# Performance work log

Hardware: AMD Instinct MI355X
Metric: run time of the kernel (lower is better)

## Reference

```python
import jax, jax.numpy as jnp
import numpy as np


def _linear_init(key, fan_in, fan_out):
    k1, k2 = jax.random.split(key)
    sc = 1.0 / np.sqrt(fan_in)
    w = jax.random.uniform(k1, (fan_in, fan_out), jnp.float32, -sc, sc)
    b = jax.random.uniform(k2, (fan_out,), jnp.float32, -sc, sc)
    return w, b


def setup_inputs() -> dict:
    key = jax.random.key(0)
    ks = jax.random.split(key, 16)
    b, s, q, c, d = 8, 5, 15, 256, 4
    inp = {
        'support_xf': jax.random.normal(ks[0], (b, s, c, d, d), jnp.float32),
        'query_xf': jax.random.normal(ks[1], (b, q, c, d, d), jnp.float32),
        'support_y': jax.random.randint(ks[2], (b, s), 0, 5),
        'query_y': jax.random.randint(ks[3], (b, q), 0, 5),
    }
    g_dims = [(516, 256), (256, 256), (256, 256), (256, 256)]
    for i, (fi, fo) in enumerate(g_dims):
        w, bb = _linear_init(ks[4 + i], fi, fo)
        inp['g_w%d' % (i + 1)] = w
        inp['g_b%d' % (i + 1)] = bb
    f_dims = [(256, 256), (256, 256), (256, 29), (29, 1)]
    for i, (fi, fo) in enumerate(f_dims):
        w, bb = _linear_init(ks[8 + i], fi, fo)
        inp['f_w%d' % (i + 1)] = w
        inp['f_b%d' % (i + 1)] = bb
    return inp


def reference(support_xf, query_xf, support_y, query_y,
              g_w1, g_b1, g_w2, g_b2, g_w3, g_b3, g_w4, g_b4,
              f_w1, f_b1, f_w2, f_b2, f_w3, f_b3, f_w4, f_b4):
    b, s, c, d, _ = support_xf.shape
    q = query_xf.shape[1]
    d2 = d * d
    relu = jax.nn.relu
    # coord channels: ch0 = i/d (row), ch1 = j/d (col), shape [2, d, d]
    ii = jnp.arange(d, dtype=support_xf.dtype) / d
    coord = jnp.stack([jnp.broadcast_to(ii[:, None], (d, d)),
                       jnp.broadcast_to(ii[None, :], (d, d))], axis=0)
    sup = jnp.concatenate([support_xf, jnp.broadcast_to(coord, (b, s, 2, d, d))], axis=2)
    qry = jnp.concatenate([query_xf, jnp.broadcast_to(coord, (b, q, 2, d, d))], axis=2)
    cp = c + 2
    sup = sup.reshape(b, s, cp, d2).transpose(0, 1, 3, 2)  # [b,s,d2,cp]
    qry = qry.reshape(b, q, cp, d2).transpose(0, 1, 3, 2)  # [b,q,d2,cp]
    # pair[b,q,s,m,n] = concat(support feature at spatial n, query feature at spatial m)
    sup_e = jnp.broadcast_to(sup[:, None, :, None, :, :], (b, q, s, d2, d2, cp))
    qry_e = jnp.broadcast_to(qry[:, :, None, :, None, :], (b, q, s, d2, d2, cp))
    x = jnp.concatenate([sup_e, qry_e], axis=-1)  # [b,q,s,d2,d2,2*cp]
    # g MLP applied per pair
    x = relu(x @ g_w1 + g_b1)
    x = relu(x @ g_w2 + g_b2)
    x = relu(x @ g_w3 + g_b3)
    x = relu(x @ g_w4 + g_b4)
    xf = x.sum(axis=(3, 4))  # sum over d^4 pairs -> [b,q,s,256]
    # f MLP (Dropout is identity in eval mode)
    y = relu(xf @ f_w1 + f_b1)
    y = relu(y @ f_w2 + f_b2)
    y = relu(y @ f_w3 + f_b3)
    score = jax.nn.sigmoid(y @ f_w4 + f_b4)[..., 0]  # [b,q,s]
    label = (support_y[:, None, :] == query_y[:, :, None]).astype(score.dtype)
    loss = jnp.sum((label - score) ** 2) / b
    return loss
```

## Files before the change

### kernel.cpp

```cpp
#include <hip/hip_runtime.h>

typedef __attribute__((ext_vector_type(8))) __bf16 bf16x8;
typedef __attribute__((ext_vector_type(8))) short short8;
typedef __attribute__((ext_vector_type(4))) float f32x4;
typedef unsigned int u32;

static __device__ __forceinline__ unsigned short f2bf(float f) {
    u32 u = __float_as_uint(f);
    u += 0x7FFFu + ((u >> 16) & 1u);
    return (unsigned short)(u >> 16);
}
static __device__ __forceinline__ u32 cvt_pk_bf16(float lo, float hi) {
    u32 r;
    asm("v_cvt_pk_bf16_f32 %0, %1, %2" : "=v"(r) : "v"(lo), "v"(hi));
    return r;
}
static __device__ __forceinline__ bf16x8 as_bf16x8(short8 v) {
    return __builtin_bit_cast(bf16x8, v);
}
static __device__ __forceinline__ f32x4 mfma16(short8 a, short8 b, f32x4 c) {
    return __builtin_amdgcn_mfma_f32_16x16x32_bf16(as_bf16x8(a), as_bf16x8(b), c, 0, 0, 0);
}

#define NB 8
#define NS 5
#define NQ 15
#define A_OFF_F 0
#define B_OFF_F (640*256)
#define XF_OFF_F (B_OFF_F + 1920*256)
#define WF_OFF_BYTES ((XF_OFF_F + 600*1024)*4)
#define WF1_OFF_BYTES (WF_OFF_BYTES + 48*8192)

__global__ void kA(const float* __restrict__ w2, const float* __restrict__ w3,
                   const float* __restrict__ w4, const float* __restrict__ w1,
                   unsigned short* __restrict__ wf, unsigned short* __restrict__ wf1) {
    int bid = blockIdx.x;
    int l = threadIdx.x;
    if (bid < 48) {
        int L = bid >> 4, tt = bid & 15;
        const float* W = (L == 0) ? w2 : ((L == 1) ? w3 : w4);
        int nn = tt * 16 + (l & 15);
        #pragma unroll
        for (int kk = 0; kk < 8; ++kk) {
            int k0 = kk * 32 + (l >> 4) * 8;
            short8 ov;
            #pragma unroll
            for (int j = 0; j < 8; ++j)
                ov[j] = (short)f2bf(W[(size_t)(k0 + j) * 256 + nn]);
            *(short8*)((char*)wf + (size_t)bid * 8192 + kk * 1024 + l * 16) = ov;
        }
        return;
    }
    int c1 = bid - 48;
    int S = c1 >> 4, tt = c1 & 15;
    int nn = tt * 16 + (l & 15);
    for (int kk = 0; kk < 9; ++kk) {
        int k0 = kk * 32 + (l >> 4) * 8;
        short8 ov;
        #pragma unroll
        for (int j = 0; j < 8; ++j) {
            int kb = k0 + j;
            float v = (kb < 258) ? w1[(size_t)(S * 258 + kb) * 256 + nn] : 0.0f;
            ov[j] = (short)f2bf(v);
        }
        *(short8*)((char*)wf1 + (size_t)c1 * 9216 + kk * 1024 + l * 16) = ov;
    }
}

__launch_bounds__(512, 1)
__global__ void kB(const float* __restrict__ sup, const float* __restrict__ qry,
                   const unsigned short* __restrict__ wf1,
                   const float* __restrict__ gb1, float* __restrict__ ws) {
    __shared__ short Xf[18432];
    int bid = blockIdx.x;
    bool isA = (bid < 10);
    int S = isA ? 0 : 1;
    int cellbase = isA ? bid * 4 : (bid - 10) * 4;
    const float* src = isA ? sup : qry;
    float* dst0 = ws + (isA ? A_OFF_F : B_OFF_F);
    int t = threadIdx.x;
    int w = t >> 6, l = t & 63;
    int g = l >> 4, c = l & 15;
    char* Xb = (char*)Xf;
    const char* w1b = (const char*)wf1;

    for (int idx = w; idx < 36; idx += 8) {
        int m = idx / 9, kk = idx % 9;
        const float* xp = src + (size_t)(cellbase + m) * 4096;
        int kbase = kk * 32 + g * 8;
        float v[8];
        #pragma unroll
        for (int j = 0; j < 8; ++j) {
            int kb = kbase + j;
            float x;
            if (kb < 256)       x = xp[(size_t)kb * 16 + c];
            else if (kb == 256) x = (float)(c >> 2) * 0.25f;
            else if (kb == 257) x = (float)(c & 3) * 0.25f;
            else                x = 0.0f;
            v[j] = x;
        }
        uint4 hv;
        hv.x = cvt_pk_bf16(v[0], v[1]);
        hv.y = cvt_pk_bf16(v[2], v[3]);
        hv.z = cvt_pk_bf16(v[4], v[5]);
        hv.w = cvt_pk_bf16(v[6], v[7]);
        *(uint4*)(Xb + (size_t)(m * 9 + kk) * 1024 + l * 16) = hv;
    }
    __syncthreads();

    int wp = w >> 2, wn = w & 3;
    const char* wbase = w1b + (size_t)(S * 16 + wn * 4) * 9216;
    short8 wcur[4];
    #pragma unroll
    for (int tti = 0; tti < 4; ++tti)
        wcur[tti] = *(const short8*)(wbase + (size_t)tti * 9216 + l * 16);

    f32x4 acc[2][4];
    #pragma unroll
    for (int pg = 0; pg < 2; ++pg)
        #pragma unroll
        for (int tti = 0; tti < 4; ++tti)
            acc[pg][tti] = (f32x4){0.f, 0.f, 0.f, 0.f};

    #pragma unroll
    for (int kk = 0; kk < 9; ++kk) {
        int kn = kk + 1; if (kn > 8) kn = 8;
        short8 wnxt[4];
        #pragma unroll
        for (int tti = 0; tti < 4; ++tti)
            wnxt[tti] = *(const short8*)(wbase + (size_t)tti * 9216 + kn * 1024 + l * 16);
        #pragma unroll
        for (int pg = 0; pg < 2; ++pg) {
            short8 h = *(const short8*)(Xb + (size_t)((wp * 2 + pg) * 9 + kk) * 1024 + l * 16);
            #pragma unroll
            for (int tti = 0; tti < 4; ++tti)
                acc[pg][tti] = mfma16(wcur[tti], h, acc[pg][tti]);
        }
        #pragma unroll
        for (int tti = 0; tti < 4; ++tti) wcur[tti] = wnxt[tti];
    }

    #pragma unroll
    for (int tti = 0; tti < 4; ++tti) {
        int col0 = wn * 64 + tti * 16 + g * 4;
        float4 bv = {0.f, 0.f, 0.f, 0.f};
        if (S == 0) bv = *(const float4*)(gb1 + col0);
        #pragma unroll
        for (int pg = 0; pg < 2; ++pg) {
            int row = (cellbase + wp * 2 + pg) * 16 + c;
            float4 o;
            o.x = acc[pg][tti][0] + bv.x;
            o.y = acc[pg][tti][1] + bv.y;
            o.z = acc[pg][tti][2] + bv.z;
            o.w = acc[pg][tti][3] + bv.w;
            *(float4*)(dst0 + (size_t)row * 256 + col0) = o;
        }
    }
}

__launch_bounds__(512, 4)
__global__ void k3_g(const float* __restrict__ wsA, const float* __restrict__ wsB,
                     const unsigned short* __restrict__ wf,
                     const float* __restrict__ gb2, const float* __restrict__ gb3,
                     const float* __restrict__ gb4, float* __restrict__ xf) {
    __shared__ short Hf[32768];
    __shared__ float bs[768];
    int bid = blockIdx.x;
    int bqs = bid >> 1, half = bid & 1;
    int b = bqs / 75, rem = bqs % 75, qi = rem / 5, si = rem % 5;
    int t = threadIdx.x;
    int w = t >> 6, l = t & 63;
    int g = l >> 4, c = l & 15;
    int wp = w >> 2, wn = w & 3;
    char* Hb = (char*)Hf;
    const char* wfb = (const char*)wf;

    if (t < 256) { bs[t] = gb2[t]; bs[256 + t] = gb3[t]; bs[512 + t] = gb4[t]; }

    short8 wcur[4];
    #pragma unroll
    for (int tti = 0; tti < 4; ++tti)
        wcur[tti] = *(const short8*)(wfb + (size_t)(wn * 4 + tti) * 8192 + l * 16);

    {
        const float* Arow = wsA + (size_t)(b * NS + si) * 4096 + c * 256;
        const float* Brow = wsB + (size_t)(b * NQ + qi) * 4096 + (half * 8 + w) * 256;
        #pragma unroll
        for (int kk = 0; kk < 8; ++kk) {
            const float* ap = Arow + kk * 32 + g * 8;
            const float* bp = Brow + kk * 32 + g * 8;
            float4 a0 = *(const float4*)ap, a1 = *(const float4*)(ap + 4);
            float4 b0 = *(const float4*)bp, b1 = *(const float4*)(bp + 4);
            uint4 hv;
            hv.x = cvt_pk_bf16(fmaxf(a0.x + b0.x, 0.f), fmaxf(a0.y + b0.y, 0.f));
            hv.y = cvt_pk_bf16(fmaxf(a0.z + b0.z, 0.f), fmaxf(a0.w + b0.w, 0.f));
            hv.z = cvt_pk_bf16(fmaxf(a1.x + b1.x, 0.f), fmaxf(a1.y + b1.y, 0.f));
            hv.w = cvt_pk_bf16(fmaxf(a1.z + b1.z, 0.f), fmaxf(a1.w + b1.w, 0.f));
            *(uint4*)(Hb + (size_t)(w * 8 + kk) * 1024 + l * 16) = hv;
        }
    }
    __syncthreads();

    #pragma unroll 1
    for (int L = 0; L < 3; ++L) {
        f32x4 acc[4][4];
        #pragma unroll
        for (int pg = 0; pg < 4; ++pg)
            #pragma unroll
            for (int tti = 0; tti < 4; ++tti)
                acc[pg][tti] = (f32x4){0.f, 0.f, 0.f, 0.f};

        #pragma unroll
        for (int kk = 0; kk < 8; ++kk) {
            int s = L * 8 + kk + 1; if (s > 23) s = 23;
            int Ln = s >> 3, kn = s & 7;
            short8 wnxt[4];
            #pragma unroll
            for (int tti = 0; tti < 4; ++tti)
                wnxt[tti] = *(const short8*)(wfb +
                    (size_t)(Ln * 16 + wn * 4 + tti) * 8192 + kn * 1024 + l * 16);
            #pragma unroll
            for (int pg = 0; pg < 4; ++pg) {
                short8 h = *(const short8*)(Hb +
                    (size_t)((wp * 4 + pg) * 8 + kk) * 1024 + l * 16);
                #pragma unroll
                for (int tti = 0; tti < 4; ++tti)
                    acc[pg][tti] = mfma16(wcur[tti], h, acc[pg][tti]);
            }
            #pragma unroll
            for (int tti = 0; tti < 4; ++tti) wcur[tti] = wnxt[tti];
        }

        float4 bv[4];
        #pragma unroll
        for (int tti = 0; tti < 4; ++tti)
            bv[tti] = *(const float4*)(bs + L * 256 + wn * 64 + tti * 16 + g * 4);

        if (L < 2) {
            __syncthreads();
            #pragma unroll
            for (int pg = 0; pg < 4; ++pg) {
                int m = wp * 4 + pg;
                #pragma unroll
                for (int tti = 0; tti < 4; ++tti) {
                    uint2 q;
                    q.x = cvt_pk_bf16(fmaxf(acc[pg][tti][0] + bv[tti].x, 0.f),
                                      fmaxf(acc[pg][tti][1] + bv[tti].y, 0.f));
                    q.y = cvt_pk_bf16(fmaxf(acc[pg][tti][2] + bv[tti].z, 0.f),
                                      fmaxf(acc[pg][tti][3] + bv[tti].w, 0.f));
                    int kk2 = wn * 2 + (tti >> 1);
                    int dlane = ((tti & 1) * 2 + (g >> 1)) * 16 + c;
                    *(uint2*)(Hb + (size_t)(m * 8 + kk2) * 1024 + dlane * 16 + (g & 1) * 8) = q;
                }
            }
            __syncthreads();
        } else {
            #pragma unroll
            for (int tti = 0; tti < 4; ++tti) {
                float s0 = 0.f, s1 = 0.f, s2 = 0.f, s3 = 0.f;
                #pragma unroll
                for (int pg = 0; pg < 4; ++pg) {
                    s0 += fmaxf(acc[pg][tti][0] + bv[tti].x, 0.f);
                    s1 += fmaxf(acc[pg][tti][1] + bv[tti].y, 0.f);
                    s2 += fmaxf(acc[pg][tti][2] + bv[tti].z, 0.f);
                    s3 += fmaxf(acc[pg][tti][3] + bv[tti].w, 0.f);
                }
                #pragma unroll
                for (int d = 1; d < 16; d <<= 1) {
                    s0 += __shfl_xor(s0, d); s1 += __shfl_xor(s1, d);
                    s2 += __shfl_xor(s2, d); s3 += __shfl_xor(s3, d);
                }
                if (c == 0) {
                    float4 o = {s0, s1, s2, s3};
                    *(float4*)(xf + (((size_t)bqs * 2 + half) * 2 + wp) * 256 +
                               wn * 64 + tti * 16 + g * 4) = o;
                }
            }
        }
    }
}

__global__ void k4_f(const float* __restrict__ xf,
                     const float* __restrict__ fw1, const float* __restrict__ fb1,
                     const float* __restrict__ fw2, const float* __restrict__ fb2,
                     const float* __restrict__ fw3, const float* __restrict__ fb3,
                     const float* __restrict__ fw4, const float* __restrict__ fb4,
                     const int* __restrict__ sy, const int* __restrict__ qy,
                     float* __restrict__ out) {
    __shared__ float xb[4][256], yb[4][256], y3[4][32];
    int base = blockIdx.x * 4;
    int t = threadIdx.x;
    #pragma unroll
    for (int cc = 0; cc < 4; ++cc) {
        const float* xr = xf + (size_t)(base + cc) * 1024 + t;
        xb[cc][t] = xr[0] + xr[256] + xr[512] + xr[768];
    }
    __syncthreads();
    float acc[4];
    #pragma unroll
    for (int cc = 0; cc < 4; ++cc) acc[cc] = fb1[t];
    #pragma unroll 8
    for (int k = 0; k < 256; ++k) {
        float wv = fw1[(size_t)k * 256 + t];
        #pragma unroll
        for (int cc = 0; cc < 4; ++cc) acc[cc] += xb[cc][k] * wv;
    }
    #pragma unroll
    for (int cc = 0; cc < 4; ++cc) yb[cc][t] = acc[cc] > 0.f ? acc[cc] : 0.f;
    __syncthreads();
    #pragma unroll
    for (int cc = 0; cc < 4; ++cc) acc[cc] = fb2[t];
    #pragma unroll 8
    for (int k = 0; k < 256; ++k) {
        float wv = fw2[(size_t)k * 256 + t];
        #pragma unroll
        for (int cc = 0; cc < 4; ++cc) acc[cc] += yb[cc][k] * wv;
    }
    #pragma unroll
    for (int cc = 0; cc < 4; ++cc) xb[cc][t] = acc[cc] > 0.f ? acc[cc] : 0.f;
    __syncthreads();
    if (t < 116) {
        int cc = t / 29, col = t % 29;
        float a = fb3[col];
        #pragma unroll 8
        for (int k = 0; k < 256; ++k) a += xb[cc][k] * fw3[(size_t)k * 29 + col];
        y3[cc][col] = a > 0.f ? a : 0.f;
    }
    __syncthreads();
    if (t < 4) {
        int cc = t;
        float z = fb4[0];
        for (int k = 0; k < 29; ++k) z += y3[cc][k] * fw4[k];
        float score = 1.0f / (1.0f + __expf(-z));
        int bqs = base + cc;
        int b = bqs / 75, rem = bqs % 75, qi = rem / 5, si = rem % 5;
        float label = (sy[b * NS + si] == qy[b * NQ + qi]) ? 1.0f : 0.0f;
        float d = label - score;
        atomicAdd(out, d * d * 0.125f);
    }
}

extern "C" void kernel_launch(void* const* d_in, const int* in_sizes, int n_in,
                              void* d_out, int out_size, void* d_ws, size_t ws_size,
                              hipStream_t stream) {
    const float* sup = (const float*)d_in[0];
    const float* qry = (const float*)d_in[1];
    const int*   sy  = (const int*)d_in[2];
    const int*   qy  = (const int*)d_in[3];
    const float* gw1 = (const float*)d_in[4];
    const float* gb1 = (const float*)d_in[5];
    const float* gw2 = (const float*)d_in[6];
    const float* gb2 = (const float*)d_in[7];
    const float* gw3 = (const float*)d_in[8];
    const float* gb3 = (const float*)d_in[9];
    const float* gw4 = (const float*)d_in[10];
    const float* gb4 = (const float*)d_in[11];
    const float* fw1 = (const float*)d_in[12];
    const float* fb1 = (const float*)d_in[13];
    const float* fw2 = (const float*)d_in[14];
    const float* fb2 = (const float*)d_in[15];
    const float* fw3 = (const float*)d_in[16];
    const float* fb3 = (const float*)d_in[17];
    const float* fw4 = (const float*)d_in[18];
    const float* fb4 = (const float*)d_in[19];

    float* ws = (float*)d_ws;
    float* A  = ws + A_OFF_F;
    float* B  = ws + B_OFF_F;
    float* xf = ws + XF_OFF_F;
    unsigned short* wf  = (unsigned short*)((char*)d_ws + WF_OFF_BYTES);
    unsigned short* wf1 = (unsigned short*)((char*)d_ws + WF1_OFF_BYTES);
    float* out = (float*)d_out;

    hipMemsetAsync(out, 0, sizeof(float), stream);

    kA<<<80, 64, 0, stream>>>(gw2, gw3, gw4, gw1, wf, wf1);
    kB<<<40, 512, 0, stream>>>(sup, qry, wf1, gb1, ws);
    k3_g<<<1200, 512, 0, stream>>>(A, B, wf, gb2, gb3, gb4, xf);
    k4_f<<<150, 256, 0, stream>>>(xf, fw1, fb1, fw2, fb2, fw3, fb3, fw4, fb4, sy, qy, out);
}
```

Before: 126.0 us.

## Split g-MLP blocks into quarters with double-buffered weights and MFMA priority

Result: no change. 127.6 us (+1.3%).

```diff
diff --git a/kernel.cpp b/kernel.cpp
--- a/kernel.cpp
+++ b/kernel.cpp
@@ -158,33 +158,55 @@
     }
 }
 
-__launch_bounds__(512, 4)
+#define K3_STEP(CUR, NXT, KK)                                                   \
+    {                                                                           \
+        int s = L * 8 + (KK) + 1; if (s > 23) s = 23;                           \
+        int Ln = s >> 3, kn = s & 7;                                            \
+        _Pragma("unroll")                                                       \
+        for (int tti = 0; tti < 4; ++tti)                                       \
+            NXT[tti] = *(const short8*)(wfb +                                   \
+                (size_t)(Ln * 16 + w * 4 + tti) * 8192 + kn * 1024 + l * 16);   \
+        short8 h0 = *(const short8*)(Hb + (size_t)(0 * 8 + (KK)) * 1024 + l * 16); \
+        short8 h1 = *(const short8*)(Hb + (size_t)(1 * 8 + (KK)) * 1024 + l * 16); \
+        short8 h2 = *(const short8*)(Hb + (size_t)(2 * 8 + (KK)) * 1024 + l * 16); \
+        short8 h3 = *(const short8*)(Hb + (size_t)(3 * 8 + (KK)) * 1024 + l * 16); \
+        __builtin_amdgcn_s_setprio(1);                                          \
+        _Pragma("unroll")                                                       \
+        for (int tti = 0; tti < 4; ++tti) {                                     \
+            acc[0][tti] = mfma16(CUR[tti], h0, acc[0][tti]);                    \
+            acc[1][tti] = mfma16(CUR[tti], h1, acc[1][tti]);                    \
+            acc[2][tti] = mfma16(CUR[tti], h2, acc[2][tti]);                    \
+            acc[3][tti] = mfma16(CUR[tti], h3, acc[3][tti]);                    \
+        }                                                                       \
+        __builtin_amdgcn_s_setprio(0);                                          \
+    }
+
+__launch_bounds__(256, 4)
 __global__ void k3_g(const float* __restrict__ wsA, const float* __restrict__ wsB,
                      const unsigned short* __restrict__ wf,
                      const float* __restrict__ gb2, const float* __restrict__ gb3,
                      const float* __restrict__ gb4, float* __restrict__ xf) {
-    __shared__ short Hf[32768];
+    __shared__ short Hf[16384];
     __shared__ float bs[768];
     int bid = blockIdx.x;
-    int bqs = bid >> 1, half = bid & 1;
+    int bqs = bid >> 2, quarter = bid & 3;
     int b = bqs / 75, rem = bqs % 75, qi = rem / 5, si = rem % 5;
     int t = threadIdx.x;
     int w = t >> 6, l = t & 63;
     int g = l >> 4, c = l & 15;
-    int wp = w >> 2, wn = w & 3;
     char* Hb = (char*)Hf;
     const char* wfb = (const char*)wf;
 
-    if (t < 256) { bs[t] = gb2[t]; bs[256 + t] = gb3[t]; bs[512 + t] = gb4[t]; }
-
-    short8 wcur[4];
+    bs[t] = gb2[t]; bs[256 + t] = gb3[t]; bs[512 + t] = gb4[t];
+
+    short8 wb0[4], wb1[4];
     #pragma unroll
     for (int tti = 0; tti < 4; ++tti)
-        wcur[tti] = *(const short8*)(wfb + (size_t)(wn * 4 + tti) * 8192 + l * 16);
+        wb0[tti] = *(const short8*)(wfb + (size_t)(w * 4 + tti) * 8192 + l * 16);
 
     {
         const float* Arow = wsA + (size_t)(b * NS + si) * 4096 + c * 256;
-        const float* Brow = wsB + (size_t)(b * NQ + qi) * 4096 + (half * 8 + w) * 256;
+        const float* Brow = wsB + (size_t)(b * NQ + qi) * 4096 + (quarter * 4 + w) * 256;
         #pragma unroll
         for (int kk = 0; kk < 8; ++kk) {
             const float* ap = Arow + kk * 32 + g * 8;
@@ -211,36 +233,20 @@
                 acc[pg][tti] = (f32x4){0.f, 0.f, 0.f, 0.f};
 
         #pragma unroll
-        for (int kk = 0; kk < 8; ++kk) {
-            int s = L * 8 + kk + 1; if (s > 23) s = 23;
-            int Ln = s >> 3, kn = s & 7;
-            short8 wnxt[4];
-            #pragma unroll
-            for (int tti = 0; tti < 4; ++tti)
-                wnxt[tti] = *(const short8*)(wfb +
-                    (size_t)(Ln * 16 + wn * 4 + tti) * 8192 + kn * 1024 + l * 16);
-            #pragma unroll
-            for (int pg = 0; pg < 4; ++pg) {
-                short8 h = *(const short8*)(Hb +
-                    (size_t)((wp * 4 + pg) * 8 + kk) * 1024 + l * 16);
-                #pragma unroll
-                for (int tti = 0; tti < 4; ++tti)
-                    acc[pg][tti] = mfma16(wcur[tti], h, acc[pg][tti]);
-            }
-            #pragma unroll
-            for (int tti = 0; tti < 4; ++tti) wcur[tti] = wnxt[tti];
+        for (int kk2 = 0; kk2 < 4; ++kk2) {
+            K3_STEP(wb0, wb1, kk2 * 2)
+            K3_STEP(wb1, wb0, kk2 * 2 + 1)
         }
 
         float4 bv[4];
         #pragma unroll
         for (int tti = 0; tti < 4; ++tti)
-            bv[tti] = *(const float4*)(bs + L * 256 + wn * 64 + tti * 16 + g * 4);
+            bv[tti] = *(const float4*)(bs + L * 256 + w * 64 + tti * 16 + g * 4);
 
         if (L < 2) {
             __syncthreads();
             #pragma unroll
             for (int pg = 0; pg < 4; ++pg) {
-                int m = wp * 4 + pg;
                 #pragma unroll
                 for (int tti = 0; tti < 4; ++tti) {
                     uint2 q;
@@ -248,9 +254,9 @@
                                       fmaxf(acc[pg][tti][1] + bv[tti].y, 0.f));
                     q.y = cvt_pk_bf16(fmaxf(acc[pg][tti][2] + bv[tti].z, 0.f),
                                       fmaxf(acc[pg][tti][3] + bv[tti].w, 0.f));
-                    int kk2 = wn * 2 + (tti >> 1);
+                    int kk2 = w * 2 + (tti >> 1);
                     int dlane = ((tti & 1) * 2 + (g >> 1)) * 16 + c;
-                    *(uint2*)(Hb + (size_t)(m * 8 + kk2) * 1024 + dlane * 16 + (g & 1) * 8) = q;
+                    *(uint2*)(Hb + (size_t)(pg * 8 + kk2) * 1024 + dlane * 16 + (g & 1) * 8) = q;
                 }
             }
             __syncthreads();
@@ -272,8 +278,8 @@
                 }
                 if (c == 0) {
                     float4 o = {s0, s1, s2, s3};
-                    *(float4*)(xf + (((size_t)bqs * 2 + half) * 2 + wp) * 256 +
-                               wn * 64 + tti * 16 + g * 4) = o;
+                    *(float4*)(xf + ((size_t)bqs * 4 + quarter) * 256 +
+                               w * 64 + tti * 16 + g * 4) = o;
                 }
             }
         }
@@ -376,6 +382,6 @@
 
     kA<<<80, 64, 0, stream>>>(gw2, gw3, gw4, gw1, wf, wf1);
     kB<<<40, 512, 0, stream>>>(sup, qry, wf1, gb1, ws);
-    k3_g<<<1200, 512, 0, stream>>>(A, B, wf, gb2, gb3, gb4, xf);
+    k3_g<<<2400, 256, 0, stream>>>(A, B, wf, gb2, gb3, gb4, xf);
     k4_f<<<150, 256, 0, stream>>>(xf, fw1, fb1, fw2, fb2, fw3, fb3, fw4, fb4, sy, qy, out);
 }
```

## Run the f-MLP head on bf16 MFMA with pre-packed weights and 64-row tiles

Applied to the files above, without the earlier changes.

After: 118.9 us. -5.6%, faster.

```diff
diff --git a/kernel.cpp b/kernel.cpp
--- a/kernel.cpp
+++ b/kernel.cpp
@@ -30,10 +30,15 @@
 #define XF_OFF_F (B_OFF_F + 1920*256)
 #define WF_OFF_BYTES ((XF_OFF_F + 600*1024)*4)
 #define WF1_OFF_BYTES (WF_OFF_BYTES + 48*8192)
+#define WFF_OFF_BYTES (WF1_OFF_BYTES + 32*9216)
+#define WF3_OFF_BYTES (WFF_OFF_BYTES + 32*8192)
 
 __global__ void kA(const float* __restrict__ w2, const float* __restrict__ w3,
                    const float* __restrict__ w4, const float* __restrict__ w1,
-                   unsigned short* __restrict__ wf, unsigned short* __restrict__ wf1) {
+                   const float* __restrict__ fw1, const float* __restrict__ fw2,
+                   const float* __restrict__ fw3,
+                   unsigned short* __restrict__ wf, unsigned short* __restrict__ wf1,
+                   unsigned short* __restrict__ wff, unsigned short* __restrict__ wf3) {
     int bid = blockIdx.x;
     int l = threadIdx.x;
     if (bid < 48) {
@@ -51,19 +56,53 @@
         }
         return;
     }
-    int c1 = bid - 48;
-    int S = c1 >> 4, tt = c1 & 15;
-    int nn = tt * 16 + (l & 15);
-    for (int kk = 0; kk < 9; ++kk) {
-        int k0 = kk * 32 + (l >> 4) * 8;
-        short8 ov;
-        #pragma unroll
-        for (int j = 0; j < 8; ++j) {
-            int kb = k0 + j;
-            float v = (kb < 258) ? w1[(size_t)(S * 258 + kb) * 256 + nn] : 0.0f;
-            ov[j] = (short)f2bf(v);
-        }
-        *(short8*)((char*)wf1 + (size_t)c1 * 9216 + kk * 1024 + l * 16) = ov;
+    if (bid < 80) {
+        int c1 = bid - 48;
+        int S = c1 >> 4, tt = c1 & 15;
+        int nn = tt * 16 + (l & 15);
+        for (int kk = 0; kk < 9; ++kk) {
+            int k0 = kk * 32 + (l >> 4) * 8;
+            short8 ov;
+            #pragma unroll
+            for (int j = 0; j < 8; ++j) {
+                int kb = k0 + j;
+                float v = (kb < 258) ? w1[(size_t)(S * 258 + kb) * 256 + nn] : 0.0f;
+                ov[j] = (short)f2bf(v);
+            }
+            *(short8*)((char*)wf1 + (size_t)c1 * 9216 + kk * 1024 + l * 16) = ov;
+        }
+        return;
+    }
+    if (bid < 112) {
+        int cid = bid - 80;
+        int Lf = cid >> 4, tt = cid & 15;
+        const float* W = (Lf == 0) ? fw1 : fw2;
+        int nn = tt * 16 + (l & 15);
+        #pragma unroll
+        for (int kk = 0; kk < 8; ++kk) {
+            int k0 = kk * 32 + (l >> 4) * 8;
+            short8 ov;
+            #pragma unroll
+            for (int j = 0; j < 8; ++j)
+                ov[j] = (short)f2bf(W[(size_t)(k0 + j) * 256 + nn]);
+            *(short8*)((char*)wff + (size_t)cid * 8192 + kk * 1024 + l * 16) = ov;
+        }
+        return;
+    }
+    {
+        int tt = bid - 112;
+        int nn = tt * 16 + (l & 15);
+        #pragma unroll
+        for (int kk = 0; kk < 8; ++kk) {
+            int k0 = kk * 32 + (l >> 4) * 8;
+            short8 ov;
+            #pragma unroll
+            for (int j = 0; j < 8; ++j) {
+                float v = (nn < 29) ? fw3[(size_t)(k0 + j) * 29 + nn] : 0.0f;
+                ov[j] = (short)f2bf(v);
+            }
+            *(short8*)((char*)wf3 + (size_t)tt * 8192 + kk * 1024 + l * 16) = ov;
+        }
     }
 }
 
@@ -280,63 +319,141 @@
     }
 }
 
+__launch_bounds__(512, 1)
 __global__ void k4_f(const float* __restrict__ xf,
-                     const float* __restrict__ fw1, const float* __restrict__ fb1,
-                     const float* __restrict__ fw2, const float* __restrict__ fb2,
-                     const float* __restrict__ fw3, const float* __restrict__ fb3,
+                     const unsigned short* __restrict__ wff,
+                     const unsigned short* __restrict__ wf3,
+                     const float* __restrict__ fb1, const float* __restrict__ fb2,
+                     const float* __restrict__ fb3,
                      const float* __restrict__ fw4, const float* __restrict__ fb4,
                      const int* __restrict__ sy, const int* __restrict__ qy,
                      float* __restrict__ out) {
-    __shared__ float xb[4][256], yb[4][256], y3[4][32];
-    int base = blockIdx.x * 4;
+    __shared__ short Hf[16384];
+    __shared__ float bs[512];
+    __shared__ float bs3[32];
+    __shared__ float y3[64][32];
+    int bid = blockIdx.x;
     int t = threadIdx.x;
+    int w = t >> 6, l = t & 63;
+    int g = l >> 4, c = l & 15;
+    char* Hb = (char*)Hf;
+    const char* wfb = (const char*)wff;
+
+    bs[t & 511] = (t < 256) ? fb1[t] : fb2[t - 256];
+    if (t < 32) bs3[t] = (t < 29) ? fb3[t] : 0.0f;
+
+    for (int fi = w; fi < 32; fi += 8) {
+        int m = fi >> 3, kk = fi & 7;
+        int row = bid * 64 + m * 16 + c;
+        if (row > 599) row = 599;
+        const float* xr = xf + (size_t)row * 1024;
+        int kb = kk * 32 + g * 8;
+        float v[8];
+        #pragma unroll
+        for (int j = 0; j < 8; ++j) {
+            int f = kb + j;
+            v[j] = xr[f] + xr[256 + f] + xr[512 + f] + xr[768 + f];
+        }
+        uint4 hv;
+        hv.x = cvt_pk_bf16(v[0], v[1]);
+        hv.y = cvt_pk_bf16(v[2], v[3]);
+        hv.z = cvt_pk_bf16(v[4], v[5]);
+        hv.w = cvt_pk_bf16(v[6], v[7]);
+        *(uint4*)(Hb + (size_t)(m * 8 + kk) * 1024 + l * 16) = hv;
+    }
+    __syncthreads();
+
+    int wp = w >> 2, wn = w & 3;
+    short8 wcur[4];
     #pragma unroll
-    for (int cc = 0; cc < 4; ++cc) {
-        const float* xr = xf + (size_t)(base + cc) * 1024 + t;
-        xb[cc][t] = xr[0] + xr[256] + xr[512] + xr[768];
+    for (int tti = 0; tti < 4; ++tti)
+        wcur[tti] = *(const short8*)(wfb + (size_t)(wn * 4 + tti) * 8192 + l * 16);
+
+    #pragma unroll 1
+    for (int L = 0; L < 2; ++L) {
+        f32x4 acc[2][4];
+        #pragma unroll
+        for (int pg = 0; pg < 2; ++pg)
+            #pragma unroll
+            for (int tti = 0; tti < 4; ++tti)
+                acc[pg][tti] = (f32x4){0.f, 0.f, 0.f, 0.f};
+
+        #pragma unroll
+        for (int kk = 0; kk < 8; ++kk) {
+            int s = L * 8 + kk + 1; if (s > 15) s = 15;
+            int Ln = s >> 3, kn = s & 7;
+            short8 wnxt[4];
+            #pragma unroll
+            for (int tti = 0; tti < 4; ++tti)
+                wnxt[tti] = *(const short8*)(wfb +
+                    (size_t)(Ln * 16 + wn * 4 + tti) * 8192 + kn * 1024 + l * 16);
+            #pragma unroll
+            for (int pg = 0; pg < 2; ++pg) {
+                short8 h = *(const short8*)(Hb +
+                    (size_t)((wp * 2 + pg) * 8 + kk) * 1024 + l * 16);
+                #pragma unroll
+                for (int tti = 0; tti < 4; ++tti)
+                    acc[pg][tti] = mfma16(wcur[tti], h, acc[pg][tti]);
+            }
+            #pragma unroll
+            for (int tti = 0; tti < 4; ++tti) wcur[tti] = wnxt[tti];
+        }
+
+        float4 bv[4];
+        #pragma unroll
+        for (int tti = 0; tti < 4; ++tti)
+            bv[tti] = *(const float4*)(bs + L * 256 + wn * 64 + tti * 16 + g * 4);
+
+        __syncthreads();
+        #pragma unroll
+        for (int pg = 0; pg < 2; ++pg) {
+            int m = wp * 2 + pg;
+            #pragma unroll
+            for (int tti = 0; tti < 4; ++tti) {
+                uint2 q;
+                q.x = cvt_pk_bf16(fmaxf(acc[pg][tti][0] + bv[tti].x, 0.f),
+                                  fmaxf(acc[pg][tti][1] + bv[tti].y, 0.f));
+                q.y = cvt_pk_bf16(fmaxf(acc[pg][tti][2] + bv[tti].z, 0.f),
+                                  fmaxf(acc[pg][tti][3] + bv[tti].w, 0.f));
+                int kk2 = wn * 2 + (tti >> 1);
+                int dlane = ((tti & 1) * 2 + (g >> 1)) * 16 + c;
+                *(uint2*)(Hb + (size_t)(m * 8 + kk2) * 1024 + dlane * 16 + (g & 1) * 8) = q;
+            }
+        }
+        __syncthreads();
+    }
+
+    {
+        int m = w >> 1, tt = w & 1;
+        f32x4 a3 = {0.f, 0.f, 0.f, 0.f};
+        #pragma unroll
+        for (int kk = 0; kk < 8; ++kk) {
+            short8 wv = *(const short8*)((const char*)wf3 +
+                (size_t)(tt * 8 + kk) * 1024 + l * 16);
+            short8 h = *(const short8*)(Hb + (size_t)(m * 8 + kk) * 1024 + l * 16);
+            a3 = mfma16(wv, h, a3);
+        }
+        #pragma unroll
+        for (int r = 0; r < 4; ++r) {
+            int oc = tt * 16 + g * 4 + r;
+            float v = a3[r] + bs3[oc];
+            y3[m * 16 + c][oc] = v > 0.f ? v : 0.f;
+        }
     }
     __syncthreads();
-    float acc[4];
-    #pragma unroll
-    for (int cc = 0; cc < 4; ++cc) acc[cc] = fb1[t];
-    #pragma unroll 8
-    for (int k = 0; k < 256; ++k) {
-        float wv = fw1[(size_t)k * 256 + t];
-        #pragma unroll
-        for (int cc = 0; cc < 4; ++cc) acc[cc] += xb[cc][k] * wv;
-    }
-    #pragma unroll
-    for (int cc = 0; cc < 4; ++cc) yb[cc][t] = acc[cc] > 0.f ? acc[cc] : 0.f;
-    __syncthreads();
-    #pragma unroll
-    for (int cc = 0; cc < 4; ++cc) acc[cc] = fb2[t];
-    #pragma unroll 8
-    for (int k = 0; k < 256; ++k) {
-        float wv = fw2[(size_t)k * 256 + t];
-        #pragma unroll
-        for (int cc = 0; cc < 4; ++cc) acc[cc] += yb[cc][k] * wv;
-    }
-    #pragma unroll
-    for (int cc = 0; cc < 4; ++cc) xb[cc][t] = acc[cc] > 0.f ? acc[cc] : 0.f;
-    __syncthreads();
-    if (t < 116) {
-        int cc = t / 29, col = t % 29;
-        float a = fb3[col];
-        #pragma unroll 8
-        for (int k = 0; k < 256; ++k) a += xb[cc][k] * fw3[(size_t)k * 29 + col];
-        y3[cc][col] = a > 0.f ? a : 0.f;
-    }
-    __syncthreads();
-    if (t < 4) {
-        int cc = t;
-        float z = fb4[0];
-        for (int k = 0; k < 29; ++k) z += y3[cc][k] * fw4[k];
-        float score = 1.0f / (1.0f + __expf(-z));
-        int bqs = base + cc;
-        int b = bqs / 75, rem = bqs % 75, qi = rem / 5, si = rem % 5;
-        float label = (sy[b * NS + si] == qy[b * NQ + qi]) ? 1.0f : 0.0f;
-        float d = label - score;
-        atomicAdd(out, d * d * 0.125f);
+
+    if (t < 64) {
+        int bqs = bid * 64 + t;
+        if (bqs < 600) {
+            float z = fb4[0];
+            #pragma unroll
+            for (int k = 0; k < 29; ++k) z += y3[t][k] * fw4[k];
+            float score = 1.0f / (1.0f + __expf(-z));
+            int b = bqs / 75, rem = bqs % 75, qi = rem / 5, si = rem % 5;
+            float label = (sy[b * NS + si] == qy[b * NQ + qi]) ? 1.0f : 0.0f;
+            float d = label - score;
+            atomicAdd(out, d * d * 0.125f);
+        }
     }
 }
 
@@ -370,12 +487,14 @@
     float* xf = ws + XF_OFF_F;
     unsigned short* wf  = (unsigned short*)((char*)d_ws + WF_OFF_BYTES);
     unsigned short* wf1 = (unsigned short*)((char*)d_ws + WF1_OFF_BYTES);
+    unsigned short* wff = (unsigned short*)((char*)d_ws + WFF_OFF_BYTES);
+    unsigned short* wf3 = (unsigned short*)((char*)d_ws + WF3_OFF_BYTES);
     float* out = (float*)d_out;
 
     hipMemsetAsync(out, 0, sizeof(float), stream);
 
-    kA<<<80, 64, 0, stream>>>(gw2, gw3, gw4, gw1, wf, wf1);
+    kA<<<114, 64, 0, stream>>>(gw2, gw3, gw4, gw1, fw1, fw2, fw3, wf, wf1, wff, wf3);
     kB<<<40, 512, 0, stream>>>(sup, qry, wf1, gb1, ws);
     k3_g<<<1200, 512, 0, stream>>>(A, B, wf, gb2, gb3, gb4, xf);
-    k4_f<<<150, 256, 0, stream>>>(xf, fw1, fb1, fw2, fb2, fw3, fb3, fw4, fb4, sy, qy, out);
-}
+    k4_f<<<10, 512, 0, stream>>>(xf, wff, wf3, fb1, fb2, fb3, fw4, fb4, sy, qy, out);
+}
```
